# Optimization experiments

Hardware: AMD Instinct MI355X
Metric: run time of the kernel (lower is better)

Reference implementation:

```python
import jax, jax.numpy as jnp
import numpy as np

WIN_H, WIN_W = 8, 16
N = WIN_H * WIN_W            # 128 tokens per window
DIM, HEADS = 512, 16
TOW = 64 // WIN_H            # type_of_windows = input_resolution[0] // window_size[0] = 8
B_WIN = 2048                 # number of windows (B_)


def _earth_position_index():
    # Faithful port of get_earth_position_index (torch wraps negative indices;
    # we pre-wrap with mod so the gather uses nonnegative indices identically).
    ch = np.arange(WIN_H)
    cw = np.arange(WIN_W)
    coords = np.stack(np.meshgrid(ch, cw, indexing='ij'))        # [2, h, w]
    cf = coords.reshape(2, -1)                                   # [2, N]
    rel = cf[:, :, None] - cf[:, None, :]                        # [2, N, N]
    rel = rel.transpose(1, 2, 0).copy()                          # [N, N, 2]
    rel[:, :, 0] *= 2 * WIN_W - 1
    rel[:, :, 1] += WIN_W - 1
    idx = rel.sum(-1)                                            # [N, N], may be negative
    table_len = WIN_H ** 2 * (2 * WIN_W - 1)                     # 1984
    return (idx % table_len).astype(np.int32)


def setup_inputs() -> dict:
    key = jax.random.key(0)
    ks = jax.random.split(key, 6)
    table_len = WIN_H ** 2 * (2 * WIN_W - 1)
    inv_sqrt_dim = 1.0 / np.sqrt(DIM)
    return {
        'x': jax.random.normal(ks[0], (B_WIN, N, DIM), dtype=jnp.float32),
        'qkv_w': jax.random.normal(ks[1], (3 * DIM, DIM), dtype=jnp.float32) * inv_sqrt_dim,
        'qkv_b': jax.random.normal(ks[2], (3 * DIM,), dtype=jnp.float32) * 0.02,
        'proj_w': jax.random.normal(ks[3], (DIM, DIM), dtype=jnp.float32) * inv_sqrt_dim,
        'proj_b': jax.random.normal(ks[4], (DIM,), dtype=jnp.float32) * 0.02,
        'bias_table': jax.random.normal(ks[5], (table_len, TOW, HEADS), dtype=jnp.float32) * 0.02,
        'pos_index': jnp.asarray(_earth_position_index()),
    }


def reference(x, qkv_w, qkv_b, proj_w, proj_b, bias_table, pos_index):
    B_, Nn, C = x.shape
    hd = C // HEADS
    scale = hd ** (-0.5)
    # fused QKV projection: [B_, N, 3, H, hd]
    qkv = (x @ qkv_w.T + qkv_b).reshape(B_, Nn, 3, HEADS, hd)
    q = qkv[:, :, 0].transpose(0, 2, 1, 3) * scale               # [B_, H, N, hd]
    k = qkv[:, :, 1].transpose(0, 2, 1, 3)
    v = qkv[:, :, 2].transpose(0, 2, 1, 3)
    attn = jnp.einsum('bhnd,bhmd->bhnm', q, k)                   # [B_, H, N, N]
    # earth position bias: gather [N*N] rows -> [N, N, TOW, H], pick middle latitude
    epb = bias_table[pos_index.reshape(-1)].reshape(Nn, Nn, TOW, HEADS)
    epb = epb[:, :, TOW // 2, :]                                 # [N, N, H]
    attn = attn + epb.transpose(2, 0, 1)[None]                   # + [1, H, N, N]
    attn = jax.nn.softmax(attn, axis=-1)
    out = jnp.einsum('bhnm,bhmd->bhnd', attn, v)                 # [B_, H, N, hd]
    out = out.transpose(0, 2, 1, 3).reshape(B_, Nn, C)
    return out @ proj_w.T + proj_b
```

## Files before the change

kernel.cpp:

```cpp
#include <hip/hip_runtime.h>
#include <hip/hip_bf16.h>


typedef short short8 __attribute__((ext_vector_type(8)));
typedef float f32x4 __attribute__((ext_vector_type(4)));
typedef unsigned short u16;
typedef unsigned int u32;

__device__ __forceinline__ u16 f2bf(float f) {
    __bf16 h = (__bf16)f;
    union { __bf16 b; u16 u; } v; v.b = h;
    return v.u;
}

__device__ __forceinline__ f32x4 mfma16(short8 a, short8 b, f32x4 c) {
    return __builtin_amdgcn_mfma_f32_16x16x32_bf16(a, b, c, 0, 0, 0);
}

#define GLDS16(gsrc, ldst)                                                  \
    __builtin_amdgcn_global_load_lds(                                       \
        (const __attribute__((address_space(1))) void*)(gsrc),              \
        (__attribute__((address_space(3))) void*)(ldst), 16, 0, 0)

__global__ __launch_bounds__(256) void cvt_x_kernel(
    const float4* __restrict__ xin, int4* __restrict__ xbf)
{
    int idx = blockIdx.x * 256 + threadIdx.x;
    for (; idx < 16777216; idx += 8192 * 256) {
        const float4 a = xin[idx * 2], b = xin[idx * 2 + 1];
        int4 o;
        o.x = (u32)f2bf(a.x) | ((u32)f2bf(a.y) << 16);
        o.y = (u32)f2bf(a.z) | ((u32)f2bf(a.w) << 16);
        o.z = (u32)f2bf(b.x) | ((u32)f2bf(b.y) << 16);
        o.w = (u32)f2bf(b.z) | ((u32)f2bf(b.w) << 16);
        xbf[idx] = o;
    }
}

__global__ __launch_bounds__(256) void prep_kernel(
    const float* __restrict__ qkv_w, const float* __restrict__ proj_w,
    const float* __restrict__ btab, const int* __restrict__ pidx,
    u16* __restrict__ qkvw_bf, u16* __restrict__ projw_bf,
    float* __restrict__ epb)
{
    const int i = blockIdx.x * 256 + threadIdx.x;
    qkvw_bf[i] = f2bf(qkv_w[i]);
    if (i < 512 * 512) projw_bf[i] = f2bf(proj_w[i]);
    if (i < 16 * 128 * 128) {
        const int rc = i & 16383, h = i >> 14;
        epb[i] = btab[pidx[rc] * 128 + 64 + h];
    }
}

template<bool EPI_QKV>
__global__ __launch_bounds__(256) void gemm_bt(
    const u16* __restrict__ A, const u16* __restrict__ Bt,
    const float* __restrict__ bias, void* __restrict__ Cv,
    const int Nn, const int K, const float qscale)
{
    __shared__ __attribute__((aligned(16))) u16 smem[2 * 128 * 64];
    u16* As = smem;
    u16* Bs = smem + 128 * 64;

    const int tid = threadIdx.x;
    const int lane = tid & 63;
    const int w = tid >> 6;
    const int lo = lane & 15, g = lane >> 4;
    const int wm = w >> 1, wn = w & 1;
    const int wu = __builtin_amdgcn_readfirstlane(w);
    const int ntile = Nn >> 7;

    int wg = blockIdx.x;
    {
        const int cpx = gridDim.x >> 3;
        wg = (wg & 7) * cpx + (wg >> 3);
    }
    const int bm = wg / ntile, bn = wg % ntile;
    const size_t m0 = (size_t)bm << 7;
    const int n0 = bn << 7;
    const int nk = K >> 6;

    const u16* pa[4];
    const u16* pb[4];
#pragma unroll
    for (int i = 0; i < 4; ++i) {
        const int s = i * 256 + tid;
        const int r = s >> 3, c16 = s & 7;
        const int csw = (c16 ^ (r & 7)) << 3;
        pa[i] = A + (m0 + r) * (size_t)K + csw;
        pb[i] = Bt + (size_t)(n0 + r) * K + csw;
    }

    f32x4 acc[4][4] = {};

#define STAGE(kt)                                                          \
    do {                                                                   \
        const int koff = (kt) * 64;                                        \
        _Pragma("unroll")                                                  \
        for (int i = 0; i < 4; ++i)                                        \
            GLDS16(pa[i] + koff, (char*)As + i * 4096 + wu * 1024);        \
        _Pragma("unroll")                                                  \
        for (int i = 0; i < 4; ++i)                                        \
            GLDS16(pb[i] + koff, (char*)Bs + i * 4096 + wu * 1024);        \
    } while (0)

    STAGE(0);
    for (int kt = 0;;) {
        __syncthreads();
#pragma unroll
        for (int kk = 0; kk < 2; ++kk) {
            short8 af[4], bq[4];
            const int cb = (kk * 4 + g) << 4;
            const int sz = (lo & 7) << 4;
#pragma unroll
            for (int i = 0; i < 4; ++i) {
                const int ra = wm * 64 + i * 16 + lo;
                af[i] = *(const short8*)((const char*)As + ((ra * 128 + cb) ^ sz));
                const int rb = wn * 64 + i * 16 + lo;
                bq[i] = *(const short8*)((const char*)Bs + ((rb * 128 + cb) ^ sz));
            }
#pragma unroll
            for (int i = 0; i < 4; ++i)
#pragma unroll
                for (int j = 0; j < 4; ++j)
                    acc[i][j] = mfma16(af[i], bq[j], acc[i][j]);
        }
        if (++kt == nk) break;
        __syncthreads();
        STAGE(kt);
    }
#undef STAGE

    if constexpr (EPI_QKV) {
        __syncthreads();
        u16* Ct = smem;
#pragma unroll
        for (int j = 0; j < 4; ++j) {
            const int c = wn * 64 + j * 16 + lo;
            const float bv = bias[n0 + c];
            const float sc = (n0 + c < 512) ? qscale : 1.0f;
#pragma unroll
            for (int i = 0; i < 4; ++i)
#pragma unroll
                for (int ii = 0; ii < 4; ++ii) {
                    const int r = wm * 64 + i * 16 + g * 4 + ii;
                    Ct[r * 128 + c] = f2bf((acc[i][j][ii] + bv) * sc);
                }
        }
        __syncthreads();
        u16* Cg = (u16*)Cv;
#pragma unroll
        for (int it = 0; it < 8; ++it) {
            const int idx = tid + it * 256;
            const int r = idx >> 4, sgm = idx & 15;
            *(int4*)(Cg + (m0 + r) * (size_t)Nn + n0 + sgm * 8) =
                *(const int4*)(Ct + r * 128 + sgm * 8);
        }
    } else {
        float* Cg = (float*)Cv;
#pragma unroll
        for (int j = 0; j < 4; ++j) {
            const int c = wn * 64 + j * 16 + lo;
            const float bv = bias[n0 + c];
#pragma unroll
            for (int i = 0; i < 4; ++i)
#pragma unroll
                for (int ii = 0; ii < 4; ++ii) {
                    const int r = wm * 64 + i * 16 + g * 4 + ii;
                    Cg[(m0 + r) * (size_t)Nn + n0 + c] = acc[i][j][ii] + bv;
                }
        }
    }
}

__global__ __launch_bounds__(256) void attn_kernel(
    const u16* __restrict__ qkv, const float* __restrict__ epb,
    u16* __restrict__ aout)
{
    __shared__ __attribute__((aligned(16))) char smem[43520];
    u16 (*Vt)[136]      = (u16(*)[136])smem;
    u16 (*Qs)[32]       = (u16(*)[32])(smem + 8704);
    u16 (*Ks)[32]       = (u16(*)[32])(smem + 16896);
    u16 (*Ps)[32][136]  = (u16(*)[32][136])(smem + 8704);
    u16 (*Os)[32]       = (u16(*)[32])smem;

    const int h = blockIdx.x >> 11;
    const int b = blockIdx.x & 2047;
    const int tid = threadIdx.x;
    const int lane = tid & 63, w = tid >> 6;
    const int lo = lane & 15, g = lane >> 4;

    const size_t base = (size_t)b * 128 * 1536 + h * 32;
#pragma unroll
    for (int it = 0; it < 2; ++it) {
        const int s = tid + it * 256;
        const int n = s >> 2, c = (s & 3) * 8;
        const u16* p = qkv + base + (size_t)n * 1536 + c;
        *(int4*)(&Qs[n][c]) = *(const int4*)(p);
        *(int4*)(&Ks[n][c]) = *(const int4*)(p + 512);
        union { int4 q; u16 u[8]; } vu;
        vu.q = *(const int4*)(p + 1024);
#pragma unroll
        for (int j = 0; j < 8; ++j) Vt[c + j][n] = vu.u[j];
    }
    __syncthreads();

    const int r0 = w * 32;

    short8 aq[2], bk[8];
    aq[0] = *(const short8*)(&Qs[r0 + lo][g * 8]);
    aq[1] = *(const short8*)(&Qs[r0 + 16 + lo][g * 8]);
#pragma unroll
    for (int j = 0; j < 8; ++j) bk[j] = *(const short8*)(&Ks[j * 16 + lo][g * 8]);

    f32x4 acc[2][8];
#pragma unroll
    for (int j = 0; j < 8; ++j) {
        f32x4 z = {0.f, 0.f, 0.f, 0.f};
        acc[0][j] = mfma16(aq[0], bk[j], z);
        acc[1][j] = mfma16(aq[1], bk[j], z);
    }

    const float* eb = epb + (h << 14);
    float mrow[2][4], rsum[2][4];
#pragma unroll
    for (int mt = 0; mt < 2; ++mt)
#pragma unroll
        for (int ii = 0; ii < 4; ++ii) { mrow[mt][ii] = -1e30f; rsum[mt][ii] = 0.f; }

#pragma unroll
    for (int mt = 0; mt < 2; ++mt)
#pragma unroll
        for (int j = 0; j < 8; ++j)
#pragma unroll
            for (int ii = 0; ii < 4; ++ii) {
                const int r = r0 + mt * 16 + g * 4 + ii;
                const int c = j * 16 + lo;
                const float sv = acc[mt][j][ii] + eb[(r << 7) + c];
                acc[mt][j][ii] = sv;
                mrow[mt][ii] = fmaxf(mrow[mt][ii], sv);
            }
#pragma unroll
    for (int d = 1; d < 16; d <<= 1)
#pragma unroll
        for (int mt = 0; mt < 2; ++mt)
#pragma unroll
            for (int ii = 0; ii < 4; ++ii)
                mrow[mt][ii] = fmaxf(mrow[mt][ii], __shfl_xor(mrow[mt][ii], d, 64));

    __syncthreads();

#pragma unroll
    for (int mt = 0; mt < 2; ++mt)
#pragma unroll
        for (int j = 0; j < 8; ++j)
#pragma unroll
            for (int ii = 0; ii < 4; ++ii) {
                const float p = __expf(acc[mt][j][ii] - mrow[mt][ii]);
                rsum[mt][ii] += p;
                Ps[w][mt * 16 + g * 4 + ii][j * 16 + lo] = f2bf(p);
            }
#pragma unroll
    for (int d = 1; d < 16; d <<= 1)
#pragma unroll
        for (int mt = 0; mt < 2; ++mt)
#pragma unroll
            for (int ii = 0; ii < 4; ++ii)
                rsum[mt][ii] += __shfl_xor(rsum[mt][ii], d, 64);

    f32x4 o[2][2] = {};
#pragma unroll
    for (int kk = 0; kk < 4; ++kk) {
        short8 av[2];
        av[0] = *(const short8*)(&Ps[w][lo][kk * 32 + g * 8]);
        av[1] = *(const short8*)(&Ps[w][16 + lo][kk * 32 + g * 8]);
#pragma unroll
        for (int dt = 0; dt < 2; ++dt) {
            const short8 bv = *(const short8*)(&Vt[dt * 16 + lo][kk * 32 + g * 8]);
            o[0][dt] = mfma16(av[0], bv, o[0][dt]);
            o[1][dt] = mfma16(av[1], bv, o[1][dt]);
        }
    }

    __syncthreads();

#pragma unroll
    for (int mt = 0; mt < 2; ++mt)
#pragma unroll
        for (int dt = 0; dt < 2; ++dt)
#pragma unroll
            for (int ii = 0; ii < 4; ++ii)
                Os[r0 + mt * 16 + g * 4 + ii][dt * 16 + lo] =
                    f2bf(o[mt][dt][ii] / rsum[mt][ii]);
    __syncthreads();

    u16* op = aout + (size_t)b * 128 * 512 + h * 32;
#pragma unroll
    for (int it = 0; it < 2; ++it) {
        const int idx = tid + it * 256;
        const int r = idx >> 2, c = (idx & 3) * 8;
        *(int4*)(op + (size_t)r * 512 + c) = *(const int4*)(&Os[r][c]);
    }
}

extern "C" void kernel_launch(void* const* d_in, const int* in_sizes, int n_in,
                              void* d_out, int out_size, void* d_ws, size_t ws_size,
                              hipStream_t stream)
{
    const float* x      = (const float*)d_in[0];
    const float* qkv_w  = (const float*)d_in[1];
    const float* qkv_b  = (const float*)d_in[2];
    const float* proj_w = (const float*)d_in[3];
    const float* proj_b = (const float*)d_in[4];
    const float* btab   = (const float*)d_in[5];
    const int*   pidx   = (const int*)d_in[6];

    char* ws = (char*)d_ws;
    u16*   xbf      = (u16*)(ws);
    u16*   attnbuf  = (u16*)(ws);
    u16*   qkvw_bf  = (u16*)(ws + 268435456);
    u16*   projw_bf = (u16*)(ws + 270008320);
    float* epb      = (float*)(ws + 270532608);
    u16*   qkvbuf   = (u16*)(ws + 271581184);

    const float qscale = 0.17677669529663687f;

    cvt_x_kernel<<<dim3(8192), dim3(256), 0, stream>>>(
        (const float4*)x, (int4*)xbf);

    prep_kernel<<<dim3(3072), dim3(256), 0, stream>>>(
        qkv_w, proj_w, btab, pidx, qkvw_bf, projw_bf, epb);

    gemm_bt<true><<<dim3(2048 * 12), dim3(256), 0, stream>>>(
        xbf, qkvw_bf, qkv_b, qkvbuf, 1536, 512, qscale);

    attn_kernel<<<dim3(32768), dim3(256), 0, stream>>>(qkvbuf, epb, attnbuf);

    gemm_bt<false><<<dim3(2048 * 4), dim3(256), 0, stream>>>(
        attnbuf, projw_bf, proj_b, d_out, 512, 512, 1.0f);
}
```

Measured before the change: 1.355 ms.

## Rewrite GEMM as 256x256 tile, 8-wave kernel with phased software pipeline

Both projection GEMMs move from 128x128 tiles with 4 waves to 256x256 tiles with 8 waves and 128KB of double-buffered LDS. The main loop is split into eight phases that interleave async global-to-LDS loads with MFMA work, using explicit barriers, waitcnt and setprio. The goal is more data reuse per tile and latency hiding for global loads, so fewer LDS stalls per MFMA. The costs are heavy LDS use (one block per CU), higher register pressure and fewer blocks in flight.

Result: slower. 1.548 ms (+14.2%).

```diff
diff --git a/kernel.cpp b/kernel.cpp
--- a/kernel.cpp
+++ b/kernel.cpp
@@ -52,23 +52,64 @@
     }
 }
 
+
+template<int BUF, int KS, int NH, int SX, int SHI, int SBUF, bool DOVM>
+__device__ __forceinline__ void gemm_phase(
+    char* sm, int aOff, int bOff, int colA,
+    short8 (&aF)[8], f32x4 (&acc)[8][4],
+    const u16* pX0, const u16* pX1, int wu1024, int st, int nk)
+{
+    short8 bF[2];
+    if constexpr (NH == 0) {
+#pragma unroll
+        for (int mi = 0; mi < 8; ++mi)
+            aF[mi] = *(const short8*)(sm + BUF * 32768 + aOff + mi * 2048 + colA);
+    }
+#pragma unroll
+    for (int j = 0; j < 2; ++j)
+        bF[j] = *(const short8*)(sm + 65536 + BUF * 32768 + bOff
+                                 + (NH * 2 + j) * 2048 + colA);
+    if (st < nk) {
+        char* d = sm + SX * 65536 + SBUF * 32768 + SHI * 16384 + wu1024;
+        const int koff = st << 6;
+        GLDS16(pX0 + koff, d);
+        GLDS16(pX1 + koff, d + 8192);
+    }
+    asm volatile("" ::: "memory");
+    __builtin_amdgcn_s_barrier();
+    asm volatile("s_waitcnt lgkmcnt(0)" ::: "memory");
+    __builtin_amdgcn_sched_barrier(0);
+    __builtin_amdgcn_s_setprio(1);
+#pragma unroll
+    for (int mi = 0; mi < 8; ++mi)
+#pragma unroll
+        for (int j = 0; j < 2; ++j)
+            acc[mi][NH * 2 + j] = mfma16(aF[mi], bF[j], acc[mi][NH * 2 + j]);
+    __builtin_amdgcn_s_setprio(0);
+    __builtin_amdgcn_sched_barrier(0);
+    if constexpr (DOVM) {
+        if (st < nk) asm volatile("s_waitcnt vmcnt(2)" ::: "memory");
+        else         asm volatile("s_waitcnt vmcnt(0)" ::: "memory");
+    }
+    asm volatile("" ::: "memory");
+    __builtin_amdgcn_s_barrier();
+}
+
 template<bool EPI_QKV>
-__global__ __launch_bounds__(256) void gemm_bt(
+__global__ __launch_bounds__(512, 2) void gemm_bt(
     const u16* __restrict__ A, const u16* __restrict__ Bt,
     const float* __restrict__ bias, void* __restrict__ Cv,
     const int Nn, const int K, const float qscale)
 {
-    __shared__ __attribute__((aligned(16))) u16 smem[2 * 128 * 64];
-    u16* As = smem;
-    u16* Bs = smem + 128 * 64;
+    __shared__ __attribute__((aligned(128))) char sm[131072];
 
     const int tid = threadIdx.x;
     const int lane = tid & 63;
     const int w = tid >> 6;
     const int lo = lane & 15, g = lane >> 4;
-    const int wm = w >> 1, wn = w & 1;
-    const int wu = __builtin_amdgcn_readfirstlane(w);
-    const int ntile = Nn >> 7;
+    const int wm = w >> 2, wn = w & 3;
+    const int wu1024 = __builtin_amdgcn_readfirstlane(w) * 1024;
+    const int ntile = Nn >> 8;
 
     int wg = blockIdx.x;
     {
@@ -76,98 +117,107 @@
         wg = (wg & 7) * cpx + (wg >> 3);
     }
     const int bm = wg / ntile, bn = wg % ntile;
-    const size_t m0 = (size_t)bm << 7;
-    const int n0 = bn << 7;
+    const size_t m0 = (size_t)bm << 8;
+    const int n0 = bn << 8;
     const int nk = K >> 6;
 
-    const u16* pa[4];
-    const u16* pb[4];
-#pragma unroll
-    for (int i = 0; i < 4; ++i) {
-        const int s = i * 256 + tid;
-        const int r = s >> 3, c16 = s & 7;
-        const int csw = (c16 ^ (r & 7)) << 3;
-        pa[i] = A + (m0 + r) * (size_t)K + csw;
-        pb[i] = Bt + (size_t)(n0 + r) * K + csw;
-    }
-
-    f32x4 acc[4][4] = {};
-
-#define STAGE(kt)                                                          \
-    do {                                                                   \
-        const int koff = (kt) * 64;                                        \
-        _Pragma("unroll")                                                  \
-        for (int i = 0; i < 4; ++i)                                        \
-            GLDS16(pa[i] + koff, (char*)As + i * 4096 + wu * 1024);        \
-        _Pragma("unroll")                                                  \
-        for (int i = 0; i < 4; ++i)                                        \
-            GLDS16(pb[i] + koff, (char*)Bs + i * 4096 + wu * 1024);        \
-    } while (0)
-
-    STAGE(0);
-    for (int kt = 0;;) {
-        __syncthreads();
-#pragma unroll
-        for (int kk = 0; kk < 2; ++kk) {
-            short8 af[4], bq[4];
-            const int cb = (kk * 4 + g) << 4;
-            const int sz = (lo & 7) << 4;
-#pragma unroll
-            for (int i = 0; i < 4; ++i) {
-                const int ra = wm * 64 + i * 16 + lo;
-                af[i] = *(const short8*)((const char*)As + ((ra * 128 + cb) ^ sz));
-                const int rb = wn * 64 + i * 16 + lo;
-                bq[i] = *(const short8*)((const char*)Bs + ((rb * 128 + cb) ^ sz));
+    const u16* pA[2][2];
+    const u16* pB[2][2];
+#pragma unroll
+    for (int round = 0; round < 2; ++round) {
+        const int rl = (round * 512 + tid) >> 3;
+        const int c16 = tid & 7;
+        const int csw = (c16 ^ (rl & 7)) << 3;
+#pragma unroll
+        for (int hi = 0; hi < 2; ++hi) {
+            pA[round][hi] = A + (m0 + hi * 128 + rl) * (size_t)K + csw;
+            pB[round][hi] = Bt + (size_t)(n0 + hi * 128 + rl) * K + csw;
+        }
+    }
+
+    const int aOff  = (wm * 128 + lo) * 128;
+    const int bOff  = (wn * 64 + lo) * 128;
+    const int colA0 = ((0 * 4 + g) ^ (lo & 7)) << 4;
+    const int colA1 = ((1 * 4 + g) ^ (lo & 7)) << 4;
+
+    short8 aF[8];
+    f32x4 acc[8][4] = {};
+
+    {
+        char* dA = sm + wu1024;
+        char* dB = sm + 65536 + wu1024;
+        GLDS16(pA[0][0], dA);          GLDS16(pA[1][0], dA + 8192);
+        GLDS16(pA[0][1], dA + 16384);  GLDS16(pA[1][1], dA + 24576);
+        GLDS16(pB[0][0], dB);          GLDS16(pB[1][0], dB + 8192);
+        GLDS16(pB[0][1], dB + 16384);  GLDS16(pB[1][1], dB + 24576);
+        char* dA1 = sm + 32768 + wu1024;
+        GLDS16(pA[0][0] + 64, dA1);    GLDS16(pA[1][0] + 64, dA1 + 8192);
+        asm volatile("s_waitcnt vmcnt(2)" ::: "memory");
+        asm volatile("" ::: "memory");
+        __builtin_amdgcn_s_barrier();
+    }
+
+    for (int t = 0; t < nk; t += 2) {
+        gemm_phase<0, 0, 0, 0, 1, 1, false>(sm, aOff, bOff, colA0, aF, acc,
+            pA[0][1], pA[1][1], wu1024, t + 1, nk);
+        gemm_phase<0, 0, 1, 1, 0, 1, false>(sm, aOff, bOff, colA0, aF, acc,
+            pB[0][0], pB[1][0], wu1024, t + 1, nk);
+        gemm_phase<0, 1, 0, 1, 1, 1, false>(sm, aOff, bOff, colA1, aF, acc,
+            pB[0][1], pB[1][1], wu1024, t + 1, nk);
+        gemm_phase<0, 1, 1, 0, 0, 0, true >(sm, aOff, bOff, colA1, aF, acc,
+            pA[0][0], pA[1][0], wu1024, t + 2, nk);
+        gemm_phase<1, 0, 0, 0, 1, 0, false>(sm, aOff, bOff, colA0, aF, acc,
+            pA[0][1], pA[1][1], wu1024, t + 2, nk);
+        gemm_phase<1, 0, 1, 1, 0, 0, false>(sm, aOff, bOff, colA0, aF, acc,
+            pB[0][0], pB[1][0], wu1024, t + 2, nk);
+        gemm_phase<1, 1, 0, 1, 1, 0, false>(sm, aOff, bOff, colA1, aF, acc,
+            pB[0][1], pB[1][1], wu1024, t + 2, nk);
+        gemm_phase<1, 1, 1, 0, 0, 1, true >(sm, aOff, bOff, colA1, aF, acc,
+            pA[0][0], pA[1][0], wu1024, t + 3, nk);
+    }
+
+    if constexpr (EPI_QKV) {
+        u16* Ct = (u16*)sm;
+        u16* Cg = (u16*)Cv;
+#pragma unroll
+        for (int p = 0; p < 2; ++p) {
+            __syncthreads();
+            if (wm == p) {
+#pragma unroll
+                for (int nj = 0; nj < 4; ++nj) {
+                    const int c = wn * 64 + nj * 16 + lo;
+                    const float bv = bias[n0 + c];
+                    const float sc = (n0 + c < 512) ? qscale : 1.0f;
+#pragma unroll
+                    for (int mi = 0; mi < 8; ++mi)
+#pragma unroll
+                        for (int ii = 0; ii < 4; ++ii) {
+                            const int r = mi * 16 + g * 4 + ii;
+                            Ct[r * 264 + c] = f2bf((acc[mi][nj][ii] + bv) * sc);
+                        }
+                }
             }
-#pragma unroll
-            for (int i = 0; i < 4; ++i)
-#pragma unroll
-                for (int j = 0; j < 4; ++j)
-                    acc[i][j] = mfma16(af[i], bq[j], acc[i][j]);
-        }
-        if (++kt == nk) break;
-        __syncthreads();
-        STAGE(kt);
-    }
-#undef STAGE
-
-    if constexpr (EPI_QKV) {
-        __syncthreads();
-        u16* Ct = smem;
-#pragma unroll
-        for (int j = 0; j < 4; ++j) {
-            const int c = wn * 64 + j * 16 + lo;
-            const float bv = bias[n0 + c];
-            const float sc = (n0 + c < 512) ? qscale : 1.0f;
-#pragma unroll
-            for (int i = 0; i < 4; ++i)
-#pragma unroll
-                for (int ii = 0; ii < 4; ++ii) {
-                    const int r = wm * 64 + i * 16 + g * 4 + ii;
-                    Ct[r * 128 + c] = f2bf((acc[i][j][ii] + bv) * sc);
-                }
-        }
-        __syncthreads();
-        u16* Cg = (u16*)Cv;
-#pragma unroll
-        for (int it = 0; it < 8; ++it) {
-            const int idx = tid + it * 256;
-            const int r = idx >> 4, sgm = idx & 15;
-            *(int4*)(Cg + (m0 + r) * (size_t)Nn + n0 + sgm * 8) =
-                *(const int4*)(Ct + r * 128 + sgm * 8);
+            __syncthreads();
+#pragma unroll
+            for (int it = 0; it < 8; ++it) {
+                const int idx = it * 512 + tid;
+                const int r = idx >> 5, seg = idx & 31;
+                *(int4*)(Cg + (m0 + p * 128 + r) * (size_t)Nn + n0 + seg * 8) =
+                    *(const int4*)(Ct + r * 264 + seg * 8);
+            }
         }
     } else {
         float* Cg = (float*)Cv;
 #pragma unroll
-        for (int j = 0; j < 4; ++j) {
-            const int c = wn * 64 + j * 16 + lo;
+        for (int nj = 0; nj < 4; ++nj) {
+            const int c = wn * 64 + nj * 16 + lo;
             const float bv = bias[n0 + c];
 #pragma unroll
-            for (int i = 0; i < 4; ++i)
+            for (int mi = 0; mi < 8; ++mi)
 #pragma unroll
                 for (int ii = 0; ii < 4; ++ii) {
-                    const int r = wm * 64 + i * 16 + g * 4 + ii;
-                    Cg[(m0 + r) * (size_t)Nn + n0 + c] = acc[i][j][ii] + bv;
+                    const size_t r = m0 + wm * 128 + mi * 16 + g * 4 + ii;
+                    Cg[r * (size_t)Nn + n0 + c] = acc[mi][nj][ii] + bv;
                 }
         }
     }
@@ -331,11 +381,11 @@
     prep_kernel<<<dim3(3072), dim3(256), 0, stream>>>(
         qkv_w, proj_w, btab, pidx, qkvw_bf, projw_bf, epb);
 
-    gemm_bt<true><<<dim3(2048 * 12), dim3(256), 0, stream>>>(
+    gemm_bt<true><<<dim3(1024 * 6), dim3(512), 0, stream>>>(
         xbf, qkvw_bf, qkv_b, qkvbuf, 1536, 512, qscale);
 
     attn_kernel<<<dim3(32768), dim3(256), 0, stream>>>(qkvbuf, epb, attnbuf);
 
-    gemm_bt<false><<<dim3(2048 * 4), dim3(256), 0, stream>>>(
+    gemm_bt<false><<<dim3(1024 * 2), dim3(512), 0, stream>>>(
         attnbuf, projw_bf, proj_b, d_out, 512, 512, 1.0f);
 }
```

## Write Q/K/V head-major with pre-transposed V and triple-buffer GEMM K-loop

Applied to the files above, without the earlier changes.

The QKV GEMM epilogue now scatters Q and K into per-(window,head) contiguous buffers and writes V already transposed, so the attention kernel can stage Q/K with direct global-to-LDS loads and V with plain vector copies instead of a strided gather plus an element-wise transpose. The GEMM main loop switches from a double-buffered 64-wide K step to a triple-buffered 32-wide K step using explicit vmcnt waits and raw barriers, dropping the XOR swizzle in LDS. This trades possible LDS bank conflicts and more barriers per K for better load/compute overlap and cheaper attention-side staging. It also uses more workspace for the three separate buffers.

Result: no change. 1.349 ms (-0.4%).

```diff
diff --git a/kernel.cpp b/kernel.cpp
--- a/kernel.cpp
+++ b/kernel.cpp
@@ -52,22 +52,22 @@
     }
 }
 
+
 template<bool EPI_QKV>
 __global__ __launch_bounds__(256) void gemm_bt(
     const u16* __restrict__ A, const u16* __restrict__ Bt,
     const float* __restrict__ bias, void* __restrict__ Cv,
+    u16* __restrict__ kb, u16* __restrict__ vtb,
     const int Nn, const int K, const float qscale)
 {
-    __shared__ __attribute__((aligned(16))) u16 smem[2 * 128 * 64];
-    u16* As = smem;
-    u16* Bs = smem + 128 * 64;
+    __shared__ __attribute__((aligned(16))) char sm[49152];
 
     const int tid = threadIdx.x;
     const int lane = tid & 63;
     const int w = tid >> 6;
     const int lo = lane & 15, g = lane >> 4;
     const int wm = w >> 1, wn = w & 1;
-    const int wu = __builtin_amdgcn_readfirstlane(w);
+    const int wofs = __builtin_amdgcn_readfirstlane(w) * 1024;
     const int ntile = Nn >> 7;
 
     int wg = blockIdx.x;
@@ -78,103 +78,129 @@
     const int bm = wg / ntile, bn = wg % ntile;
     const size_t m0 = (size_t)bm << 7;
     const int n0 = bn << 7;
-    const int nk = K >> 6;
-
-    const u16* pa[4];
-    const u16* pb[4];
-#pragma unroll
-    for (int i = 0; i < 4; ++i) {
-        const int s = i * 256 + tid;
-        const int r = s >> 3, c16 = s & 7;
-        const int csw = (c16 ^ (r & 7)) << 3;
-        pa[i] = A + (m0 + r) * (size_t)K + csw;
-        pb[i] = Bt + (size_t)(n0 + r) * K + csw;
-    }
+    const int nk = K >> 5;
+
+    const int slot = w * 64 + lane;
+    const int rs = slot >> 2, c8 = (slot & 3) * 8;
+    const u16* pa0 = A + (m0 + rs) * (size_t)K + c8;
+    const u16* pa1 = pa0 + (size_t)64 * K;
+    const u16* pb0 = Bt + (size_t)(n0 + rs) * K + c8;
+    const u16* pb1 = pb0 + (size_t)64 * K;
+
+#define STAGE(buf, kt)                                                     \
+    do {                                                                   \
+        const int ko = (kt) << 5;                                          \
+        char* d = sm + (buf) * 16384 + wofs;                               \
+        GLDS16(pa0 + ko, d);                                               \
+        GLDS16(pa1 + ko, d + 4096);                                        \
+        GLDS16(pb0 + ko, d + 8192);                                        \
+        GLDS16(pb1 + ko, d + 12288);                                       \
+    } while (0)
 
     f32x4 acc[4][4] = {};
 
-#define STAGE(kt)                                                          \
-    do {                                                                   \
-        const int koff = (kt) * 64;                                        \
-        _Pragma("unroll")                                                  \
-        for (int i = 0; i < 4; ++i)                                        \
-            GLDS16(pa[i] + koff, (char*)As + i * 4096 + wu * 1024);        \
-        _Pragma("unroll")                                                  \
-        for (int i = 0; i < 4; ++i)                                        \
-            GLDS16(pb[i] + koff, (char*)Bs + i * 4096 + wu * 1024);        \
-    } while (0)
-
-    STAGE(0);
-    for (int kt = 0;;) {
-        __syncthreads();
-#pragma unroll
-        for (int kk = 0; kk < 2; ++kk) {
-            short8 af[4], bq[4];
-            const int cb = (kk * 4 + g) << 4;
-            const int sz = (lo & 7) << 4;
-#pragma unroll
-            for (int i = 0; i < 4; ++i) {
-                const int ra = wm * 64 + i * 16 + lo;
-                af[i] = *(const short8*)((const char*)As + ((ra * 128 + cb) ^ sz));
-                const int rb = wn * 64 + i * 16 + lo;
-                bq[i] = *(const short8*)((const char*)Bs + ((rb * 128 + cb) ^ sz));
-            }
-#pragma unroll
-            for (int i = 0; i < 4; ++i)
-#pragma unroll
-                for (int j = 0; j < 4; ++j)
-                    acc[i][j] = mfma16(af[i], bq[j], acc[i][j]);
+    STAGE(0, 0);
+    STAGE(1, 1);
+    asm volatile("s_waitcnt vmcnt(4)" ::: "memory");
+    __builtin_amdgcn_s_barrier();
+
+    int cur = 0, pre = 2;
+    for (int t = 0; t < nk; ++t) {
+        if (t + 2 < nk) STAGE(pre, t + 2);
+        const char* Ab = sm + cur * 16384;
+        const char* Bb = Ab + 8192;
+        short8 af[4], bq[4];
+#pragma unroll
+        for (int i = 0; i < 4; ++i) {
+            af[i] = *(const short8*)(Ab + (wm * 64 + i * 16 + lo) * 64 + g * 16);
+            bq[i] = *(const short8*)(Bb + (wn * 64 + i * 16 + lo) * 64 + g * 16);
         }
-        if (++kt == nk) break;
-        __syncthreads();
-        STAGE(kt);
+#pragma unroll
+        for (int i = 0; i < 4; ++i)
+#pragma unroll
+            for (int j = 0; j < 4; ++j)
+                acc[i][j] = mfma16(af[i], bq[j], acc[i][j]);
+        if (t + 2 < nk) asm volatile("s_waitcnt vmcnt(4)" ::: "memory");
+        else            asm volatile("s_waitcnt vmcnt(0)" ::: "memory");
+        asm volatile("" ::: "memory");
+        __builtin_amdgcn_s_barrier();
+        cur = (cur == 2) ? 0 : cur + 1;
+        pre = (pre == 2) ? 0 : pre + 1;
     }
 #undef STAGE
 
     if constexpr (EPI_QKV) {
-        __syncthreads();
-        u16* Ct = smem;
+        u16* Ct = (u16*)sm;
+        const int b16 = ((int)(m0 >> 7)) * 16;
+        const int tsel = bn >> 2;
+        const int h0 = (bn & 3) << 2;
+        u16* outb = (tsel == 0) ? (u16*)Cv : (tsel == 1) ? kb : vtb;
+        if (tsel < 2) {
+            const float sc = (tsel == 0) ? qscale : 1.0f;
+#pragma unroll
+            for (int j = 0; j < 4; ++j) {
+                const int c = wn * 64 + j * 16 + lo;
+                const float bv = bias[n0 + c];
+#pragma unroll
+                for (int i = 0; i < 4; ++i)
+#pragma unroll
+                    for (int ii = 0; ii < 4; ++ii) {
+                        const int r = wm * 64 + i * 16 + g * 4 + ii;
+                        Ct[r * 136 + c] = f2bf((acc[i][j][ii] + bv) * sc);
+                    }
+            }
+            __syncthreads();
+#pragma unroll
+            for (int it = 0; it < 8; ++it) {
+                const int idx = it * 256 + tid;
+                const int r = idx >> 4, s2 = idx & 15;
+                const int hl = s2 >> 2, d0 = (s2 & 3) * 8;
+                *(int4*)(outb + ((size_t)(b16 + h0 + hl) * 128 + r) * 32 + d0) =
+                    *(const int4*)(Ct + r * 136 + s2 * 8);
+            }
+        } else {
+#pragma unroll
+            for (int j = 0; j < 4; ++j) {
+                const int c = wn * 64 + j * 16 + lo;
+                const float bv = bias[n0 + c];
+#pragma unroll
+                for (int i = 0; i < 4; ++i)
+#pragma unroll
+                    for (int ii = 0; ii < 4; ++ii) {
+                        const int r = wm * 64 + i * 16 + g * 4 + ii;
+                        Ct[c * 136 + r] = f2bf(acc[i][j][ii] + bv);
+                    }
+            }
+            __syncthreads();
+#pragma unroll
+            for (int it = 0; it < 8; ++it) {
+                const int idx = it * 256 + tid;
+                const int cidx = idx >> 4, nc = idx & 15;
+                const int hl = cidx >> 5, d = cidx & 31;
+                *(int4*)(outb + ((size_t)(b16 + h0 + hl) * 32 + d) * 128 + nc * 8) =
+                    *(const int4*)(Ct + cidx * 136 + nc * 8);
+            }
+        }
+    } else {
+        float* Cg = (float*)Cv;
 #pragma unroll
         for (int j = 0; j < 4; ++j) {
             const int c = wn * 64 + j * 16 + lo;
             const float bv = bias[n0 + c];
-            const float sc = (n0 + c < 512) ? qscale : 1.0f;
 #pragma unroll
             for (int i = 0; i < 4; ++i)
 #pragma unroll
                 for (int ii = 0; ii < 4; ++ii) {
-                    const int r = wm * 64 + i * 16 + g * 4 + ii;
-                    Ct[r * 128 + c] = f2bf((acc[i][j][ii] + bv) * sc);
+                    const size_t r = m0 + wm * 64 + i * 16 + g * 4 + ii;
+                    Cg[r * (size_t)Nn + n0 + c] = acc[i][j][ii] + bv;
                 }
         }
-        __syncthreads();
-        u16* Cg = (u16*)Cv;
-#pragma unroll
-        for (int it = 0; it < 8; ++it) {
-            const int idx = tid + it * 256;
-            const int r = idx >> 4, sgm = idx & 15;
-            *(int4*)(Cg + (m0 + r) * (size_t)Nn + n0 + sgm * 8) =
-                *(const int4*)(Ct + r * 128 + sgm * 8);
-        }
-    } else {
-        float* Cg = (float*)Cv;
-#pragma unroll
-        for (int j = 0; j < 4; ++j) {
-            const int c = wn * 64 + j * 16 + lo;
-            const float bv = bias[n0 + c];
-#pragma unroll
-            for (int i = 0; i < 4; ++i)
-#pragma unroll
-                for (int ii = 0; ii < 4; ++ii) {
-                    const int r = wm * 64 + i * 16 + g * 4 + ii;
-                    Cg[(m0 + r) * (size_t)Nn + n0 + c] = acc[i][j][ii] + bv;
-                }
-        }
     }
 }
 
 __global__ __launch_bounds__(256) void attn_kernel(
-    const u16* __restrict__ qkv, const float* __restrict__ epb,
+    const u16* __restrict__ qbuf, const u16* __restrict__ kbuf,
+    const u16* __restrict__ vtbuf, const float* __restrict__ epb,
     u16* __restrict__ aout)
 {
     __shared__ __attribute__((aligned(16))) char smem[43520];
@@ -189,19 +215,25 @@
     const int tid = threadIdx.x;
     const int lane = tid & 63, w = tid >> 6;
     const int lo = lane & 15, g = lane >> 4;
-
-    const size_t base = (size_t)b * 128 * 1536 + h * 32;
+    const int wu = __builtin_amdgcn_readfirstlane(w);
+
+    const size_t hb = (size_t)(b * 16 + h) * 4096;
+    const u16* qp = qbuf + hb;
+    const u16* kp = kbuf + hb;
+    const u16* vp = vtbuf + hb;
+
+#pragma unroll
+    for (int cc = 0; cc < 2; ++cc) {
+        const int ch = wu * 2 + cc;
+        GLDS16(qp + ch * 512 + lane * 8, (char*)Qs + ch * 1024);
+        GLDS16(kp + ch * 512 + lane * 8, (char*)Ks + ch * 1024);
+    }
 #pragma unroll
     for (int it = 0; it < 2; ++it) {
-        const int s = tid + it * 256;
-        const int n = s >> 2, c = (s & 3) * 8;
-        const u16* p = qkv + base + (size_t)n * 1536 + c;
-        *(int4*)(&Qs[n][c]) = *(const int4*)(p);
-        *(int4*)(&Ks[n][c]) = *(const int4*)(p + 512);
-        union { int4 q; u16 u[8]; } vu;
-        vu.q = *(const int4*)(p + 1024);
-#pragma unroll
-        for (int j = 0; j < 8; ++j) Vt[c + j][n] = vu.u[j];
+        const int idx = tid + it * 256;
+        const int d = idx >> 4, nc = idx & 15;
+        const int4 v = *(const int4*)(vp + idx * 8);
+        *(int4*)(&Vt[d][nc * 8]) = v;
     }
     __syncthreads();
 
@@ -321,7 +353,9 @@
     u16*   qkvw_bf  = (u16*)(ws + 268435456);
     u16*   projw_bf = (u16*)(ws + 270008320);
     float* epb      = (float*)(ws + 270532608);
-    u16*   qkvbuf   = (u16*)(ws + 271581184);
+    u16*   qbuf     = (u16*)(ws + 271581184);
+    u16*   kbuf     = (u16*)(ws + 540016640);
+    u16*   vtbuf    = (u16*)(ws + 808452096);
 
     const float qscale = 0.17677669529663687f;
 
@@ -332,10 +366,11 @@
         qkv_w, proj_w, btab, pidx, qkvw_bf, projw_bf, epb);
 
     gemm_bt<true><<<dim3(2048 * 12), dim3(256), 0, stream>>>(
-        xbf, qkvw_bf, qkv_b, qkvbuf, 1536, 512, qscale);
-
-    attn_kernel<<<dim3(32768), dim3(256), 0, stream>>>(qkvbuf, epb, attnbuf);
+        xbf, qkvw_bf, qkv_b, qbuf, kbuf, vtbuf, 1536, 512, qscale);
+
+    attn_kernel<<<dim3(32768), dim3(256), 0, stream>>>(
+        qbuf, kbuf, vtbuf, epb, attnbuf);
 
     gemm_bt<false><<<dim3(2048 * 4), dim3(256), 0, stream>>>(
-        attnbuf, projw_bf, proj_b, d_out, 512, 512, 1.0f);
-}
+        attnbuf, projw_bf, proj_b, d_out, nullptr, nullptr, 512, 512, 1.0f);
+}
```
